# Performance work log

Measured on AMD Instinct MI355X. Metric: run time of the kernel, lower is better.

## Reference

```python
import jax, jax.numpy as jnp
import numpy as np

T, D, E, K = 16384, 2048, 64, 2
LOAD_BALANCE_SCALE = 0.01
NOISY_STD = 1.0


def setup_inputs() -> dict:
    key = jax.random.key(0)
    k1, k2, k3, k4 = jax.random.split(key, 4)
    x_flat = jax.random.normal(k1, (T, D), dtype=jnp.float32)
    noise = jax.random.normal(k2, (T, E), dtype=jnp.float32)
    # gate_linear: nn.Linear(D, E, bias=False) -> weight [E, D]
    W_gate = jax.random.normal(k3, (E, D), dtype=jnp.float32) * (1.0 / np.sqrt(D))
    # noise_weight initialized to zeros in torch; use small values so the
    # noisy path is exercised numerically.
    noise_weight = jax.random.normal(k4, (E,), dtype=jnp.float32) * 0.01
    return {"x_flat": x_flat, "noise": noise, "W_gate": W_gate,
            "noise_weight": noise_weight, "k": K}


def reference(x_flat, noise, W_gate, noise_weight, k):
    # logits = x @ W^T   [T, E]
    logits = jnp.einsum("td,ed->te", x_flat, W_gate)
    logits_noisy = logits + (noise * NOISY_STD) * noise_weight

    # noisy top-k; softmax over -inf-sparse logits == softmax over the k
    # selected logits scattered into zeros (top-k ids are unique per row).
    top_vals, top_ids = jax.lax.top_k(logits_noisy, k)          # [T, k]
    gates_k = jax.nn.softmax(top_vals, axis=-1)                 # [T, k]
    rows = jnp.arange(x_flat.shape[0])[:, None]
    top_k_gated_weights = jnp.zeros_like(logits_noisy).at[rows, top_ids].set(gates_k)

    # load-balance loss on clean logits
    gate_weights_mean = jax.nn.softmax(logits, axis=-1).mean(axis=0)  # [E]
    uniform = jnp.full_like(gate_weights_mean, 1.0 / gate_weights_mean.shape[0])
    load_balance_loss = jnp.mean((gate_weights_mean - uniform) ** 2) * LOAD_BALANCE_SCALE

    return top_k_gated_weights, top_ids, load_balance_loss
```

## Files before the change

kernel.cpp:

```cpp
#include <hip/hip_runtime.h>
#include <hip/hip_bf16.h>

#define T_TOK 16384
#define D_DIM 2048
#define E_EXP 64
#define TAU   2e-3f

typedef __bf16 bf16x8 __attribute__((ext_vector_type(8)));
typedef float  f32x16 __attribute__((ext_vector_type(16)));

#define WS_WHI  0
#define WS_WLO  (256*1024)
#define WS_SUM  (512*1024)
#define WS_CNT  (512*1024 + 512)
#define WS_FLG  (512*1024 + 1024)

__device__ __forceinline__ unsigned short bf16_rne(float x){
  unsigned int u = __float_as_uint(x);
  return (unsigned short)((u + 0x7FFFu + ((u >> 16) & 1u)) >> 16);
}

__device__ __forceinline__ void ins3(float& v1, int& i1, float& v2, int& i2,
                                     float& v3, int& i3, float v, int i){
  if (v > v1 || (v == v1 && i < i1)) { v3=v2; i3=i2; v2=v1; i2=i1; v1=v; i1=i; }
  else if (v > v2 || (v == v2 && i < i2)) { v3=v2; i3=i2; v2=v; i2=i; }
  else if (v > v3 || (v == v3 && i < i3)) { v3=v; i3=i; }
}

__global__ void wsplit_kernel(const float* __restrict__ W,
                              unsigned short* __restrict__ whi,
                              unsigned short* __restrict__ wlo){
  int i = blockIdx.x * 256 + threadIdx.x;
  float x = W[i];
  unsigned short h = bf16_rne(x);
  whi[i] = h;
  wlo[i] = bf16_rne(x - __uint_as_float(((unsigned int)h) << 16));
}

__launch_bounds__(256, 2)
__global__ void moe_main(const float* __restrict__ X, const float* __restrict__ NZ,
                         const unsigned short* __restrict__ WHI,
                         const unsigned short* __restrict__ WLO,
                         const float* __restrict__ NW, float* __restrict__ OUT,
                         double* __restrict__ ESUM, int* __restrict__ FCNT,
                         int* __restrict__ FLIST)
{
  __shared__ __align__(16) char smem[49152];

  const int tid  = threadIdx.x;
  const int lane = tid & 63;
  const int wv   = tid >> 6;
  const int nt   = wv & 1;
  const int kh   = wv >> 1;
  const int r0   = blockIdx.x << 5;
  const int m    = lane & 31;
  const int kg   = lane >> 5;
  const int ex   = nt*32 + m;

  const int sr = tid >> 3, sc = tid & 7;
  const int we = tid >> 2, wp = tid & 3;

  const float*          xg  = X   + (size_t)(r0 + sr)*D_DIM + sc*8;
  const unsigned short* whg = WHI + (size_t)we*D_DIM + wp*16;
  const unsigned short* wlg = WLO + (size_t)we*D_DIM + wp*16;

  const int xw_hi = sr*128 + ((sc ^ (sr & 7)) << 4);
  const int ww_g0 = ((wp*2)     ^ (we & 7)) << 4;
  const int ww_g1 = ((wp*2 + 1) ^ (we & 7)) << 4;
  const int ww_row = we*128;

  f32x16 acc;
  #pragma unroll
  for (int i = 0; i < 16; ++i) acc[i] = 0.0f;

  float4 xa, xb; uint4 wh0, wh1, wl0, wl1;

  #define LOAD_CHUNK(c) do {                                                   \
    xa  = *reinterpret_cast<const float4*>(xg  + (c)*64);                      \
    xb  = *reinterpret_cast<const float4*>(xg  + (c)*64 + 4);                  \
    wh0 = *reinterpret_cast<const uint4*>(whg + (c)*64);                       \
    wh1 = *reinterpret_cast<const uint4*>(whg + (c)*64 + 8);                   \
    wl0 = *reinterpret_cast<const uint4*>(wlg + (c)*64);                       \
    wl1 = *reinterpret_cast<const uint4*>(wlg + (c)*64 + 8);                   \
  } while(0)

  #define WRITE_CHUNK(bufbase) do {                                            \
    char* Bp = smem + (bufbase);                                               \
    float f0=xa.x, f1=xa.y, f2=xa.z, f3=xa.w, f4=xb.x, f5=xb.y, f6=xb.z, f7=xb.w; \
    unsigned short h0=bf16_rne(f0),h1=bf16_rne(f1),h2=bf16_rne(f2),h3=bf16_rne(f3); \
    unsigned short h4=bf16_rne(f4),h5=bf16_rne(f5),h6=bf16_rne(f6),h7=bf16_rne(f7); \
    uint4 hv, lv;                                                              \
    hv.x = h0 | ((unsigned)h1<<16); hv.y = h2 | ((unsigned)h3<<16);            \
    hv.z = h4 | ((unsigned)h5<<16); hv.w = h6 | ((unsigned)h7<<16);            \
    lv.x = bf16_rne(f0-__uint_as_float((unsigned)h0<<16)) |                    \
           ((unsigned)bf16_rne(f1-__uint_as_float((unsigned)h1<<16))<<16);     \
    lv.y = bf16_rne(f2-__uint_as_float((unsigned)h2<<16)) |                    \
           ((unsigned)bf16_rne(f3-__uint_as_float((unsigned)h3<<16))<<16);     \
    lv.z = bf16_rne(f4-__uint_as_float((unsigned)h4<<16)) |                    \
           ((unsigned)bf16_rne(f5-__uint_as_float((unsigned)h5<<16))<<16);     \
    lv.w = bf16_rne(f6-__uint_as_float((unsigned)h6<<16)) |                    \
           ((unsigned)bf16_rne(f7-__uint_as_float((unsigned)h7<<16))<<16);     \
    *reinterpret_cast<uint4*>(Bp + xw_hi)          = hv;                       \
    *reinterpret_cast<uint4*>(Bp + 4096 + xw_hi)   = lv;                       \
    *reinterpret_cast<uint4*>(Bp + 8192  + ww_row + ww_g0) = wh0;              \
    *reinterpret_cast<uint4*>(Bp + 8192  + ww_row + ww_g1) = wh1;              \
    *reinterpret_cast<uint4*>(Bp + 16384 + ww_row + ww_g0) = wl0;              \
    *reinterpret_cast<uint4*>(Bp + 16384 + ww_row + ww_g1) = wl1;              \
  } while(0)

  LOAD_CHUNK(0);
  WRITE_CHUNK(0);
  __syncthreads();

  #pragma unroll 2
  for (int c = 0; c < 32; ++c){
    const int bufbase = (c & 1) * 24576;
    if (c < 31) LOAD_CHUNK(c + 1);
    {
      const char* Bp = smem + bufbase;
      #pragma unroll
      for (int ks2 = 0; ks2 < 2; ++ks2){
        const int ks = kh*2 + ks2;
        const int g0 = ks*2 + kg;
        bf16x8 ah = *reinterpret_cast<const bf16x8*>(Bp +         m*128  + ((g0 ^ (m  & 7)) << 4));
        bf16x8 al = *reinterpret_cast<const bf16x8*>(Bp + 4096  + m*128  + ((g0 ^ (m  & 7)) << 4));
        bf16x8 bh = *reinterpret_cast<const bf16x8*>(Bp + 8192  + ex*128 + ((g0 ^ (ex & 7)) << 4));
        bf16x8 bl = *reinterpret_cast<const bf16x8*>(Bp + 16384 + ex*128 + ((g0 ^ (ex & 7)) << 4));
        acc = __builtin_amdgcn_mfma_f32_32x32x16_bf16(ah, bh, acc, 0, 0, 0);
        acc = __builtin_amdgcn_mfma_f32_32x32x16_bf16(ah, bl, acc, 0, 0, 0);
        acc = __builtin_amdgcn_mfma_f32_32x32x16_bf16(al, bh, acc, 0, 0, 0);
      }
    }
    if (c < 31) WRITE_CHUNK((c & 1) ? 0 : 24576);
    __syncthreads();
  }
  #undef LOAD_CHUNK
  #undef WRITE_CHUNK

  float* lgts = (float*)(smem);
  float* nzs  = (float*)(smem + 8192);
  float* prb  = (float*)(smem + 16384);
  float* nws  = (float*)(smem + 24576);

  if (kh == 0){
    #pragma unroll
    for (int r = 0; r < 16; ++r){
      int rr = (r & 3) + ((r >> 2) << 3) + (kg << 2);
      lgts[rr*64 + ex] = acc[r];
    }
  }
  __syncthreads();
  if (kh == 1){
    #pragma unroll
    for (int r = 0; r < 16; ++r){
      int rr = (r & 3) + ((r >> 2) << 3) + (kg << 2);
      lgts[rr*64 + ex] += acc[r];
    }
  }
  {
    *reinterpret_cast<float4*>(&nzs[sr*64 + sc*8]) =
      *reinterpret_cast<const float4*>(NZ + (size_t)(r0 + sr)*E_EXP + sc*8);
    *reinterpret_cast<float4*>(&nzs[sr*64 + sc*8 + 4]) =
      *reinterpret_cast<const float4*>(NZ + (size_t)(r0 + sr)*E_EXP + sc*8 + 4);
  }
  if (tid < 64) nws[tid] = NW[tid];
  __syncthreads();

  {
    const int rrow = (wv << 3) + (lane >> 3);
    const int j    = lane & 7;
    const int trow = r0 + rrow;
    float cl[8];
    float v1 = -INFINITY, v2 = -INFINITY, v3 = -INFINITY;
    int   i1 = 1 << 29,   i2 = 1 << 29,   i3 = 1 << 29;
    #pragma unroll
    for (int mm = 0; mm < 8; ++mm){
      int q = j + (mm << 3);
      float lg = lgts[rrow*64 + q];
      cl[mm] = lg;
      float vn = fmaf(nzs[rrow*64 + q], nws[q], lg);
      ins3(v1,i1,v2,i2,v3,i3, vn, q);
    }
    #pragma unroll
    for (int d = 1; d < 8; d <<= 1){
      float ov1 = __shfl_xor(v1, d, 8), ov2 = __shfl_xor(v2, d, 8), ov3 = __shfl_xor(v3, d, 8);
      int   oi1 = __shfl_xor(i1, d, 8), oi2 = __shfl_xor(i2, d, 8), oi3 = __shfl_xor(i3, d, 8);
      ins3(v1,i1,v2,i2,v3,i3, ov1, oi1);
      ins3(v1,i1,v2,i2,v3,i3, ov2, oi2);
      ins3(v1,i1,v2,i2,v3,i3, ov3, oi3);
    }
    float e1 = expf(v2 - v1);
    float g0 = 1.0f / (1.0f + e1);
    float g1 = e1 * g0;

    float mx = cl[0];
    #pragma unroll
    for (int mm = 1; mm < 8; ++mm) mx = fmaxf(mx, cl[mm]);
    #pragma unroll
    for (int d = 1; d < 8; d <<= 1) mx = fmaxf(mx, __shfl_xor(mx, d, 8));
    float sum = 0.0f, exv[8];
    #pragma unroll
    for (int mm = 0; mm < 8; ++mm){ exv[mm] = expf(cl[mm] - mx); sum += exv[mm]; }
    #pragma unroll
    for (int d = 1; d < 8; d <<= 1) sum += __shfl_xor(sum, d, 8);
    float inv = 1.0f / sum;
    #pragma unroll
    for (int mm = 0; mm < 8; ++mm) prb[rrow*64 + j + (mm << 3)] = exv[mm] * inv;

    if (j == 0){
      OUT[(size_t)T_TOK*E_EXP + (size_t)trow*2]     = (float)i1;
      OUT[(size_t)T_TOK*E_EXP + (size_t)trow*2 + 1] = (float)i2;
      if ((v1 - v2 < TAU) || (v2 - v3 < TAU)){
        int slot = atomicAdd(FCNT, 1);
        FLIST[slot] = trow;
      }
    }
    #pragma unroll
    for (int mm = 0; mm < 8; ++mm){
      int q = j + (mm << 3);
      lgts[rrow*64 + q] = (q == i1) ? g0 : ((q == i2) ? g1 : 0.0f);
    }
  }
  __syncthreads();

  {
    *reinterpret_cast<float4*>(OUT + (size_t)(r0 + sr)*E_EXP + sc*8) =
      *reinterpret_cast<const float4*>(&lgts[sr*64 + sc*8]);
    *reinterpret_cast<float4*>(OUT + (size_t)(r0 + sr)*E_EXP + sc*8 + 4) =
      *reinterpret_cast<const float4*>(&lgts[sr*64 + sc*8 + 4]);
  }
  if (tid < 64){
    float s0 = 0.0f;
    #pragma unroll 8
    for (int rr2 = 0; rr2 < 32; ++rr2) s0 += prb[rr2*64 + tid];
    atomicAdd(&ESUM[tid], (double)s0);
  }
}

__launch_bounds__(256)
__global__ void moe_fixup(const float* __restrict__ X, const float* __restrict__ NZ,
                          const float* __restrict__ WG, const float* __restrict__ NW,
                          float* __restrict__ OUT, const int* __restrict__ FCNT,
                          const int* __restrict__ FLIST)
{
  __shared__ __align__(16) float xl[2048];
  __shared__ double lz[64];
  __shared__ int   si1, si2;
  __shared__ float sg0, sg1;
  const int n    = *FCNT;
  const int lane = threadIdx.x & 63;
  const int wv   = threadIdx.x >> 6;
  for (int idx = blockIdx.x; idx < n; idx += gridDim.x){
    const int t = FLIST[idx];
    {
      int off = threadIdx.x * 8;
      *reinterpret_cast<float4*>(xl + off) =
        *reinterpret_cast<const float4*>(X + (size_t)t*D_DIM + off);
      *reinterpret_cast<float4*>(xl + off + 4) =
        *reinterpret_cast<const float4*>(X + (size_t)t*D_DIM + off + 4);
    }
    __syncthreads();
    for (int s = 0; s < 16; ++s){
      const int e = wv*16 + s;
      const float* wr = WG + (size_t)e*D_DIM;
      double acc = 0.0;
      #pragma unroll
      for (int it = 0; it < 8; ++it){
        float4 w4 = *reinterpret_cast<const float4*>(wr + it*256 + lane*4);
        float4 x4 = *reinterpret_cast<const float4*>(xl + it*256 + lane*4);
        acc += (double)x4.x * (double)w4.x;
        acc += (double)x4.y * (double)w4.y;
        acc += (double)x4.z * (double)w4.z;
        acc += (double)x4.w * (double)w4.w;
      }
      #pragma unroll
      for (int off = 1; off < 64; off <<= 1) acc += __shfl_xor(acc, off, 64);
      if (lane == 0)
        lz[e] = acc + (double)NZ[(size_t)t*E_EXP + e] * (double)NW[e];
    }
    __syncthreads();
    if (threadIdx.x == 0){
      double b1 = -1e300, b2 = -1e300; int j1 = 0, j2 = 0;
      for (int q = 0; q < 64; ++q){
        double v = lz[q];
        if (v > b1){ b2 = b1; j2 = j1; b1 = v; j1 = q; }
        else if (v > b2){ b2 = v; j2 = q; }
      }
      double ee = exp(b2 - b1);
      sg0 = (float)(1.0 / (1.0 + ee));
      sg1 = (float)(ee / (1.0 + ee));
      si1 = j1; si2 = j2;
      OUT[(size_t)T_TOK*E_EXP + (size_t)t*2]     = (float)j1;
      OUT[(size_t)T_TOK*E_EXP + (size_t)t*2 + 1] = (float)j2;
    }
    __syncthreads();
    if (threadIdx.x < 64)
      OUT[(size_t)t*E_EXP + threadIdx.x] = (threadIdx.x == si1) ? sg0 :
                                           ((threadIdx.x == si2) ? sg1 : 0.0f);
    __syncthreads();
  }
}

__global__ void moe_loss(const double* __restrict__ ESUM, float* __restrict__ OUT){
  const int e = threadIdx.x;
  double d = ESUM[e] * (1.0 / T_TOK) - (1.0 / 64.0);
  double sq = d * d;
  #pragma unroll
  for (int off = 1; off < 64; off <<= 1) sq += __shfl_xor(sq, off, 64);
  if (e == 0) OUT[(size_t)T_TOK*E_EXP + T_TOK*2] = (float)(sq * (0.01 / 64.0));
}

extern "C" void kernel_launch(void* const* d_in, const int* in_sizes, int n_in,
                              void* d_out, int out_size, void* d_ws, size_t ws_size,
                              hipStream_t stream)
{
  const float* X  = (const float*)d_in[0];
  const float* NZ = (const float*)d_in[1];
  const float* WG = (const float*)d_in[2];
  const float* NW = (const float*)d_in[3];
  float* OUT = (float*)d_out;
  char*  ws  = (char*)d_ws;
  unsigned short* WHI = (unsigned short*)(ws + WS_WHI);
  unsigned short* WLO = (unsigned short*)(ws + WS_WLO);
  double* ESUM = (double*)(ws + WS_SUM);
  int* FCNT  = (int*)(ws + WS_CNT);
  int* FLIST = (int*)(ws + WS_FLG);

  hipMemsetAsync(ws + WS_SUM, 0, 1024, stream);
  wsplit_kernel<<<dim3(512), dim3(256), 0, stream>>>(WG, WHI, WLO);
  moe_main<<<dim3(T_TOK/32), dim3(256), 0, stream>>>(X, NZ, WHI, WLO, NW, OUT, ESUM, FCNT, FLIST);
  moe_fixup<<<dim3(512), dim3(256), 0, stream>>>(X, NZ, WG, NW, OUT, FCNT, FLIST);
  moe_loss<<<dim3(1), dim3(64), 0, stream>>>(ESUM, OUT);
}
```

Baseline: 118.8 us.

## Stream GEMM operands via global_load_lds into triple-buffered LDS pipeline

```diff
diff --git a/kernel.cpp b/kernel.cpp
--- a/kernel.cpp
+++ b/kernel.cpp
@@ -8,6 +8,7 @@
 
 typedef __bf16 bf16x8 __attribute__((ext_vector_type(8)));
 typedef float  f32x16 __attribute__((ext_vector_type(16)));
+typedef unsigned short ushort_t;
 
 #define WS_WHI  0
 #define WS_WLO  (256*1024)
@@ -27,25 +28,48 @@
   else if (v > v3 || (v == v3 && i < i3)) { v3=v; i3=i; }
 }
 
+__device__ __forceinline__ void gload16(const void* g, const void* l){
+  __builtin_amdgcn_global_load_lds(
+      (const __attribute__((address_space(1))) unsigned int*)g,
+      (__attribute__((address_space(3))) unsigned int*)l, 16, 0, 0);
+}
+
 __global__ void wsplit_kernel(const float* __restrict__ W,
-                              unsigned short* __restrict__ whi,
-                              unsigned short* __restrict__ wlo){
-  int i = blockIdx.x * 256 + threadIdx.x;
-  float x = W[i];
-  unsigned short h = bf16_rne(x);
-  whi[i] = h;
-  wlo[i] = bf16_rne(x - __uint_as_float(((unsigned int)h) << 16));
+                              ushort_t* __restrict__ whi, ushort_t* __restrict__ wlo,
+                              double* __restrict__ ESUM, int* __restrict__ FCNT){
+  const int n = blockIdx.x * 256 + threadIdx.x;
+  if (blockIdx.x == 0){
+    if (threadIdx.x < 64) ESUM[threadIdx.x] = 0.0;
+    else if (threadIdx.x == 64) *FCNT = 0;
+  }
+  const int c = n >> 9, s = n & 511;
+  const int grp = s >> 6, l = s & 63;
+  const int ks = grp >> 1, nt = grp & 1;
+  const int m = l & 31, kg = l >> 5;
+  const float* src = W + (size_t)(nt*32 + m)*D_DIM + c*64 + ks*16 + kg*8;
+  float4 w0 = *reinterpret_cast<const float4*>(src);
+  float4 w1 = *reinterpret_cast<const float4*>(src + 4);
+  float f[8] = {w0.x,w0.y,w0.z,w0.w,w1.x,w1.y,w1.z,w1.w};
+  unsigned h[8], lo[8];
+  #pragma unroll
+  for (int i = 0; i < 8; ++i){
+    h[i]  = bf16_rne(f[i]);
+    lo[i] = bf16_rne(f[i] - __uint_as_float(h[i] << 16));
+  }
+  uint4 hv = { h[0]|(h[1]<<16),  h[2]|(h[3]<<16),  h[4]|(h[5]<<16),  h[6]|(h[7]<<16) };
+  uint4 lv = { lo[0]|(lo[1]<<16), lo[2]|(lo[3]<<16), lo[4]|(lo[5]<<16), lo[6]|(lo[7]<<16) };
+  *reinterpret_cast<uint4*>(whi + (size_t)n*8) = hv;
+  *reinterpret_cast<uint4*>(wlo + (size_t)n*8) = lv;
 }
 
 __launch_bounds__(256, 2)
 __global__ void moe_main(const float* __restrict__ X, const float* __restrict__ NZ,
-                         const unsigned short* __restrict__ WHI,
-                         const unsigned short* __restrict__ WLO,
+                         const ushort_t* __restrict__ WHI, const ushort_t* __restrict__ WLO,
                          const float* __restrict__ NW, float* __restrict__ OUT,
                          double* __restrict__ ESUM, int* __restrict__ FCNT,
                          int* __restrict__ FLIST)
 {
-  __shared__ __align__(16) char smem[49152];
+  __shared__ __align__(16) char smem[73728];
 
   const int tid  = threadIdx.x;
   const int lane = tid & 63;
@@ -55,92 +79,87 @@
   const int r0   = blockIdx.x << 5;
   const int m    = lane & 31;
   const int kg   = lane >> 5;
-  const int ex   = nt*32 + m;
-
-  const int sr = tid >> 3, sc = tid & 7;
-  const int we = tid >> 2, wp = tid & 3;
-
-  const float*          xg  = X   + (size_t)(r0 + sr)*D_DIM + sc*8;
-  const unsigned short* whg = WHI + (size_t)we*D_DIM + wp*16;
-  const unsigned short* wlg = WLO + (size_t)we*D_DIM + wp*16;
-
-  const int xw_hi = sr*128 + ((sc ^ (sr & 7)) << 4);
-  const int ww_g0 = ((wp*2)     ^ (we & 7)) << 4;
-  const int ww_g1 = ((wp*2 + 1) ^ (we & 7)) << 4;
-  const int ww_row = we*128;
+
+  const int ga  = wv*64 + lane;
+  const int rA  = ga >> 4, gxp = ga & 15;
+  const int gxA = gxp ^ (rA & 15);
+  const char* px0 = (const char*)X + ((size_t)(r0 + rA)*D_DIM + gxA*4) * 4;
+  const char* px1 = px0 + (size_t)16*D_DIM*4;
+  const char* pwh = (const char*)WHI + (size_t)(wv*64 + lane)*16;
+  const char* pwl = (const char*)WLO + (size_t)(wv*64 + lane)*16;
 
   f32x16 acc;
   #pragma unroll
   for (int i = 0; i < 16; ++i) acc[i] = 0.0f;
 
-  float4 xa, xb; uint4 wh0, wh1, wl0, wl1;
-
-  #define LOAD_CHUNK(c) do {                                                   \
-    xa  = *reinterpret_cast<const float4*>(xg  + (c)*64);                      \
-    xb  = *reinterpret_cast<const float4*>(xg  + (c)*64 + 4);                  \
-    wh0 = *reinterpret_cast<const uint4*>(whg + (c)*64);                       \
-    wh1 = *reinterpret_cast<const uint4*>(whg + (c)*64 + 8);                   \
-    wl0 = *reinterpret_cast<const uint4*>(wlg + (c)*64);                       \
-    wl1 = *reinterpret_cast<const uint4*>(wlg + (c)*64 + 8);                   \
-  } while(0)
-
-  #define WRITE_CHUNK(bufbase) do {                                            \
-    char* Bp = smem + (bufbase);                                               \
-    float f0=xa.x, f1=xa.y, f2=xa.z, f3=xa.w, f4=xb.x, f5=xb.y, f6=xb.z, f7=xb.w; \
-    unsigned short h0=bf16_rne(f0),h1=bf16_rne(f1),h2=bf16_rne(f2),h3=bf16_rne(f3); \
-    unsigned short h4=bf16_rne(f4),h5=bf16_rne(f5),h6=bf16_rne(f6),h7=bf16_rne(f7); \
-    uint4 hv, lv;                                                              \
-    hv.x = h0 | ((unsigned)h1<<16); hv.y = h2 | ((unsigned)h3<<16);            \
-    hv.z = h4 | ((unsigned)h5<<16); hv.w = h6 | ((unsigned)h7<<16);            \
-    lv.x = bf16_rne(f0-__uint_as_float((unsigned)h0<<16)) |                    \
-           ((unsigned)bf16_rne(f1-__uint_as_float((unsigned)h1<<16))<<16);     \
-    lv.y = bf16_rne(f2-__uint_as_float((unsigned)h2<<16)) |                    \
-           ((unsigned)bf16_rne(f3-__uint_as_float((unsigned)h3<<16))<<16);     \
-    lv.z = bf16_rne(f4-__uint_as_float((unsigned)h4<<16)) |                    \
-           ((unsigned)bf16_rne(f5-__uint_as_float((unsigned)h5<<16))<<16);     \
-    lv.w = bf16_rne(f6-__uint_as_float((unsigned)h6<<16)) |                    \
-           ((unsigned)bf16_rne(f7-__uint_as_float((unsigned)h7<<16))<<16);     \
-    *reinterpret_cast<uint4*>(Bp + xw_hi)          = hv;                       \
-    *reinterpret_cast<uint4*>(Bp + 4096 + xw_hi)   = lv;                       \
-    *reinterpret_cast<uint4*>(Bp + 8192  + ww_row + ww_g0) = wh0;              \
-    *reinterpret_cast<uint4*>(Bp + 8192  + ww_row + ww_g1) = wh1;              \
-    *reinterpret_cast<uint4*>(Bp + 16384 + ww_row + ww_g0) = wl0;              \
-    *reinterpret_cast<uint4*>(Bp + 16384 + ww_row + ww_g1) = wl1;              \
-  } while(0)
-
-  LOAD_CHUNK(0);
-  WRITE_CHUNK(0);
-  __syncthreads();
-
-  #pragma unroll 2
-  for (int c = 0; c < 32; ++c){
-    const int bufbase = (c & 1) * 24576;
-    if (c < 31) LOAD_CHUNK(c + 1);
-    {
-      const char* Bp = smem + bufbase;
-      #pragma unroll
-      for (int ks2 = 0; ks2 < 2; ++ks2){
-        const int ks = kh*2 + ks2;
-        const int g0 = ks*2 + kg;
-        bf16x8 ah = *reinterpret_cast<const bf16x8*>(Bp +         m*128  + ((g0 ^ (m  & 7)) << 4));
-        bf16x8 al = *reinterpret_cast<const bf16x8*>(Bp + 4096  + m*128  + ((g0 ^ (m  & 7)) << 4));
-        bf16x8 bh = *reinterpret_cast<const bf16x8*>(Bp + 8192  + ex*128 + ((g0 ^ (ex & 7)) << 4));
-        bf16x8 bl = *reinterpret_cast<const bf16x8*>(Bp + 16384 + ex*128 + ((g0 ^ (ex & 7)) << 4));
-        acc = __builtin_amdgcn_mfma_f32_32x32x16_bf16(ah, bh, acc, 0, 0, 0);
-        acc = __builtin_amdgcn_mfma_f32_32x32x16_bf16(ah, bl, acc, 0, 0, 0);
-        acc = __builtin_amdgcn_mfma_f32_32x32x16_bf16(al, bh, acc, 0, 0, 0);
-      }
-    }
-    if (c < 31) WRITE_CHUNK((c & 1) ? 0 : 24576);
-    __syncthreads();
-  }
-  #undef LOAD_CHUNK
-  #undef WRITE_CHUNK
+  #define ISSUE(c, Boff) do{                                                   \
+    const size_t xo = (size_t)(c)*256, wo = (size_t)(c)*8192;                  \
+    gload16(px0 + xo,        smem + (Boff) +          wv*1024);                \
+    gload16(px1 + xo,        smem + (Boff) +       (wv+4)*1024);               \
+    gload16(pwh + wo,        smem + (Boff) + 8192  +  wv*1024);                \
+    gload16(pwh + wo + 4096, smem + (Boff) + 8192  + (wv+4)*1024);             \
+    gload16(pwl + wo,        smem + (Boff) + 16384 +  wv*1024);                \
+    gload16(pwl + wo + 4096, smem + (Boff) + 16384 + (wv+4)*1024);             \
+  }while(0)
+
+  #define COMPUTE(Boff) do{                                                    \
+    const char* Bp = smem + (Boff);                                            \
+    _Pragma("unroll")                                                          \
+    for (int ks2 = 0; ks2 < 2; ++ks2){                                         \
+      const int ks = kh*2 + ks2;                                               \
+      float4 fa = *reinterpret_cast<const float4*>(Bp + m*256 + (((ks*4+kg*2  ) ^ (m&15))<<4)); \
+      float4 fb = *reinterpret_cast<const float4*>(Bp + m*256 + (((ks*4+kg*2+1) ^ (m&15))<<4)); \
+      bf16x8 bh = *reinterpret_cast<const bf16x8*>(Bp + 8192  + ((((ks<<1)|nt)<<10) | (lane<<4))); \
+      bf16x8 bl = *reinterpret_cast<const bf16x8*>(Bp + 16384 + ((((ks<<1)|nt)<<10) | (lane<<4))); \
+      float fv[8] = {fa.x,fa.y,fa.z,fa.w,fb.x,fb.y,fb.z,fb.w};                 \
+      bf16x8 ah, al;                                                           \
+      _Pragma("unroll")                                                        \
+      for (int ii = 0; ii < 8; ++ii){                                          \
+        __bf16 hh = (__bf16)fv[ii];                                            \
+        ah[ii] = hh; al[ii] = (__bf16)(fv[ii] - (float)hh);                    \
+      }                                                                        \
+      acc = __builtin_amdgcn_mfma_f32_32x32x16_bf16(ah, bh, acc, 0, 0, 0);     \
+      acc = __builtin_amdgcn_mfma_f32_32x32x16_bf16(ah, bl, acc, 0, 0, 0);     \
+      acc = __builtin_amdgcn_mfma_f32_32x32x16_bf16(al, bh, acc, 0, 0, 0);     \
+    }                                                                          \
+  }while(0)
+
+  #define WAITV(n) do{ asm volatile("s_waitcnt vmcnt(" #n ")" ::: "memory");   \
+                       __builtin_amdgcn_sched_barrier(0); }while(0)
+
+  ISSUE(0, 0); ISSUE(1, 24576); ISSUE(2, 49152);
+
+  #pragma unroll 1
+  for (int g = 0; g < 10; ++g){
+    const int c = g*3;
+    WAITV(12); __builtin_amdgcn_s_barrier();
+    COMPUTE(0);
+    __builtin_amdgcn_s_barrier();
+    if (c < 29) ISSUE(c+3, 0);
+    WAITV(12); __builtin_amdgcn_s_barrier();
+    COMPUTE(24576);
+    __builtin_amdgcn_s_barrier();
+    if (c+1 < 29) ISSUE(c+4, 24576);
+    WAITV(12); __builtin_amdgcn_s_barrier();
+    COMPUTE(49152);
+    __builtin_amdgcn_s_barrier();
+    if (c+2 < 29) ISSUE(c+5, 49152);
+  }
+  WAITV(6);  __builtin_amdgcn_s_barrier();
+  COMPUTE(0);
+  __builtin_amdgcn_s_barrier();
+  WAITV(0);  __builtin_amdgcn_s_barrier();
+  COMPUTE(24576);
+
+  #undef ISSUE
+  #undef COMPUTE
+  #undef WAITV
 
   float* lgts = (float*)(smem);
   float* nzs  = (float*)(smem + 8192);
   float* prb  = (float*)(smem + 16384);
-  float* nws  = (float*)(smem + 24576);
+  float* nws  = (float*)(smem + 49152);
+  const int ex = nt*32 + m;
 
   if (kh == 0){
     #pragma unroll
@@ -157,6 +176,7 @@
       lgts[rr*64 + ex] += acc[r];
     }
   }
+  const int sr = tid >> 3, sc = tid & 7;
   {
     *reinterpret_cast<float4*>(&nzs[sr*64 + sc*8]) =
       *reinterpret_cast<const float4*>(NZ + (size_t)(r0 + sr)*E_EXP + sc*8);
@@ -320,14 +340,13 @@
   const float* NW = (const float*)d_in[3];
   float* OUT = (float*)d_out;
   char*  ws  = (char*)d_ws;
-  unsigned short* WHI = (unsigned short*)(ws + WS_WHI);
-  unsigned short* WLO = (unsigned short*)(ws + WS_WLO);
+  ushort_t* WHI = (ushort_t*)(ws + WS_WHI);
+  ushort_t* WLO = (ushort_t*)(ws + WS_WLO);
   double* ESUM = (double*)(ws + WS_SUM);
   int* FCNT  = (int*)(ws + WS_CNT);
   int* FLIST = (int*)(ws + WS_FLG);
 
-  hipMemsetAsync(ws + WS_SUM, 0, 1024, stream);
-  wsplit_kernel<<<dim3(512), dim3(256), 0, stream>>>(WG, WHI, WLO);
+  wsplit_kernel<<<dim3(64), dim3(256), 0, stream>>>(WG, WHI, WLO, ESUM, FCNT);
   moe_main<<<dim3(T_TOK/32), dim3(256), 0, stream>>>(X, NZ, WHI, WLO, NW, OUT, ESUM, FCNT, FLIST);
   moe_fixup<<<dim3(512), dim3(256), 0, stream>>>(X, NZ, WG, NW, OUT, FCNT, FLIST);
   moe_loss<<<dim3(1), dim3(64), 0, stream>>>(ESUM, OUT);
```

New measurement: 114.4 us. -3.8%, faster.
